# Optimization experiments

Measured on AMD Instinct MI355X. Metric: run time of the kernel, lower is better.

## Reference

```python
import jax, jax.numpy as jnp
import numpy as np

B, T, C, H = 4, 2048, 1024, 16


def setup_inputs() -> dict:
    key = jax.random.key(0)
    ks = jax.random.split(key, 5)
    s_attn = 1.0 / np.sqrt(C)
    s_proj = 1.0 / np.sqrt(C)
    return {
        "x": jax.random.normal(ks[0], (B, T, C), dtype=jnp.float32),
        "w_attn": jax.random.uniform(ks[1], (3 * C, C), dtype=jnp.float32, minval=-s_attn, maxval=s_attn),
        "b_attn": jax.random.uniform(ks[2], (3 * C,), dtype=jnp.float32, minval=-s_attn, maxval=s_attn),
        "w_proj": jax.random.uniform(ks[3], (C, C), dtype=jnp.float32, minval=-s_proj, maxval=s_proj),
        "b_proj": jax.random.uniform(ks[4], (C,), dtype=jnp.float32, minval=-s_proj, maxval=s_proj),
    }


def reference(x, w_attn, b_attn, w_proj, b_proj):
    b, t, c = x.shape
    hd = c // H  # head dim
    qkv = jnp.einsum('btc,dc->btd', x, w_attn) + b_attn  # [B,T,3C]
    q, k, v = jnp.split(qkv, 3, axis=-1)
    # [B,H,T,hd]
    q = q.reshape(b, t, H, hd).transpose(0, 2, 1, 3)
    k = k.reshape(b, t, H, hd).transpose(0, 2, 1, 3)
    v = v.reshape(b, t, H, hd).transpose(0, 2, 1, 3)
    att = jnp.einsum('bhqd,bhkd->bhqk', q, k) * (1.0 / np.sqrt(hd))
    mask = jnp.tril(jnp.ones((t, t), dtype=bool))  # causal
    att = jnp.where(mask, att, -jnp.inf)
    att = jax.nn.softmax(att, axis=-1)
    y = jnp.einsum('bhqk,bhkd->bhqd', att, v)
    y = y.transpose(0, 2, 1, 3).reshape(b, t, c)
    return jnp.einsum('btc,dc->btd', y, w_proj) + b_proj
```

## Files before the change

### kernel.cpp

```cpp
#include <hip/hip_runtime.h>

#define Bb 4
#define Tt 2048
#define Cc 1024
#define Hh 16
#define NQKV 3072
#define Mtot 8192

typedef __bf16 bf16_t;
typedef unsigned short u16;
typedef __bf16 bf16x8 __attribute__((ext_vector_type(8)));
typedef __bf16 bf16x4 __attribute__((ext_vector_type(4)));
typedef short short4v __attribute__((ext_vector_type(4)));
typedef float f32x4 __attribute__((ext_vector_type(4)));
typedef float f32x16 __attribute__((ext_vector_type(16)));
typedef unsigned uint2v __attribute__((ext_vector_type(2)));

union bfu { bf16_t b; u16 u; };
union trpair { short4v h[2]; bf16x8 v; };
union pfu { unsigned u[4]; bf16x8 v; };

#define QSCALE 0.18033688011112042f

#define TRD(dst, addr, OFF)                                                     \
  asm volatile("ds_read_b64_tr_b16 %0, %1 offset:" OFF                          \
               : "=v"(dst) : "v"(addr) : "memory")

__device__ __forceinline__ unsigned cvtpk(float a, float b) {
  unsigned r;
  asm("v_cvt_pk_bf16_f32 %0, %1, %2" : "=v"(r) : "v"(a), "v"(b));
  return r;
}
__device__ __forceinline__ uint2v plswap(unsigned a, unsigned b) {
  return __builtin_amdgcn_permlane32_swap(a, b, false, false);
}

__device__ __forceinline__ void cvt8(const float* s, u16* d, size_t i, float f) {
  float4 a = *(const float4*)(s + i);
  float4 b = *(const float4*)(s + i + 4);
  bf16x8 v;
  v[0]=(bf16_t)(a.x*f); v[1]=(bf16_t)(a.y*f); v[2]=(bf16_t)(a.z*f); v[3]=(bf16_t)(a.w*f);
  v[4]=(bf16_t)(b.x*f); v[5]=(bf16_t)(b.y*f); v[6]=(bf16_t)(b.z*f); v[7]=(bf16_t)(b.w*f);
  *(bf16x8*)(d + i) = v;
}

__global__ __launch_bounds__(256) void cvt_all(
    const float* __restrict__ x, const float* __restrict__ w_attn,
    const float* __restrict__ w_proj, const float* __restrict__ b_attn,
    u16* __restrict__ xb, u16* __restrict__ wab, u16* __restrict__ wpb,
    float* __restrict__ sbias)
{
  const int blk = blockIdx.x;
  if (blk < 4096) {
    size_t i = ((size_t)blk * 256 + threadIdx.x) * 8;
    cvt8(x, xb, i, 1.0f);
  } else if (blk < 5632) {
    size_t i = ((size_t)(blk - 4096) * 256 + threadIdx.x) * 8;
    cvt8(w_attn, wab, i, (i < (size_t)Cc * Cc) ? QSCALE : 1.0f);
  } else if (blk < 6144) {
    size_t i = ((size_t)(blk - 5632) * 256 + threadIdx.x) * 8;
    cvt8(w_proj, wpb, i, 1.0f);
  } else {
    int i0 = (blk - 6144) * 2048 + threadIdx.x * 8;
#pragma unroll
    for (int j = 0; j < 8; ++j) {
      int i = i0 + j;
      if (i < NQKV) sbias[i] = b_attn[i] * ((i < Cc) ? QSCALE : 1.0f);
    }
  }
}

template <int OUTBF16>
__global__ __launch_bounds__(256) void gemm_bf16(
    const u16* __restrict__ A, const u16* __restrict__ Bm,
    const float* __restrict__ bias, void* __restrict__ Cout,
    int M, int N, int K)
{
  __shared__ __attribute__((aligned(16))) u16 sa[128][40];
  __shared__ __attribute__((aligned(16))) u16 sb[128][40];

  const int tid  = threadIdx.x;
  const int lane = tid & 63;
  const int wid  = tid >> 6;
  const int wr   = (wid >> 1) * 64;
  const int wc   = (wid & 1) * 64;
  const int l15  = lane & 15;
  const int lh   = lane >> 4;
  const int bm   = blockIdx.x * 128;
  const int bn   = blockIdx.y * 128;

  f32x4 acc[4][4] = {};

  const int srow = tid >> 1;
  const int sseg = (tid & 1) * 16;

  const u16* pa = A  + (size_t)(bm + srow) * K + sseg;
  const u16* pb = Bm + (size_t)(bn + srow) * K + sseg;

  uint4 ar0 = *(const uint4*)pa, ar1 = *(const uint4*)(pa + 8);
  uint4 br0 = *(const uint4*)pb, br1 = *(const uint4*)(pb + 8);
  pa += 32; pb += 32;

  for (int k0 = 0; k0 < K; k0 += 32) {
    __syncthreads();
    *(uint4*)&sa[srow][sseg]     = ar0;
    *(uint4*)&sa[srow][sseg + 8] = ar1;
    *(uint4*)&sb[srow][sseg]     = br0;
    *(uint4*)&sb[srow][sseg + 8] = br1;
    __syncthreads();
    if (k0 + 32 < K) {
      ar0 = *(const uint4*)pa; ar1 = *(const uint4*)(pa + 8);
      br0 = *(const uint4*)pb; br1 = *(const uint4*)(pb + 8);
      pa += 32; pb += 32;
    }
    bf16x8 af[4], bfv[4];
#pragma unroll
    for (int mi = 0; mi < 4; mi++)
      af[mi] = *(const bf16x8*)&sa[wr + mi*16 + l15][lh * 8];
#pragma unroll
    for (int ni = 0; ni < 4; ni++)
      bfv[ni] = *(const bf16x8*)&sb[wc + ni*16 + l15][lh * 8];
#pragma unroll
    for (int mi = 0; mi < 4; mi++)
#pragma unroll
      for (int ni = 0; ni < 4; ni++)
        acc[mi][ni] = __builtin_amdgcn_mfma_f32_16x16x32_bf16(
            af[mi], bfv[ni], acc[mi][ni], 0, 0, 0);
  }

#pragma unroll
  for (int mi = 0; mi < 4; mi++) {
#pragma unroll
    for (int ni = 0; ni < 4; ni++) {
      const int col = bn + wc + ni*16 + l15;
      const float bs = bias[col];
#pragma unroll
      for (int r = 0; r < 4; r++) {
        const int row = bm + wr + mi*16 + lh*4 + r;
        const float val = acc[mi][ni][r] + bs;
        if (OUTBF16) {
          bfu cv; cv.b = (bf16_t)val;
          ((u16*)Cout)[(size_t)row * N + col] = cv.u;
        } else {
          ((float*)Cout)[(size_t)row * N + col] = val;
        }
      }
    }
  }
}

#define BUFU 9216

__global__ __launch_bounds__(512) void attn_kernel(
    const u16* __restrict__ qkv, u16* __restrict__ y)
{
  __shared__ __attribute__((aligned(16))) u16 smem[3 * BUFU];

  const int tid  = threadIdx.x;
  const int lane = tid & 63;
  const int w    = tid >> 6;
  const int l31  = lane & 31;
  const int hh   = lane >> 5;
  const int l15  = lane & 15;
  const int lh   = lane >> 4;
  const int bh   = blockIdx.y;
  const int b    = bh >> 4;
  const int head = bh & 15;

  const size_t rowbase = (size_t)b * Tt * NQKV;

  const int skey = tid >> 3;
  const int sp   = tid & 7;
  const u16* kbase = qkv + rowbase + 1024 + head*64 + sp*8;
  const u16* vbase = qkv + rowbase + 2048 + head*64 + sp*8;

  const unsigned smemB = (unsigned)(size_t)(&smem[0]);
  const unsigned trl = smemB
      + ((lh>>1)*8 + (l15>>2))*144 + (lh&1)*32 + (l15&3)*8;

  uint4 kr0, vr0;
#define LOADREGS(t) do {                                                        \
    kr0 = *(const uint4*)(kbase + (size_t)((t)*64 + skey) * NQKV);              \
    vr0 = *(const uint4*)(vbase + (size_t)((t)*64 + skey) * NQKV);              \
  } while (0)
#define STAGEB(bofs) do {                                                       \
    *(uint4*)&smem[(bofs) + skey*72 + sp*8]        = kr0;                       \
    *(uint4*)&smem[(bofs) + 4608 + skey*72 + sp*8] = vr0;                       \
  } while (0)

  for (int half = 0; half < 2; ++half) {
    const int qx    = half ? (7 - (int)blockIdx.x) : (int)blockIdx.x;
    const int qbase = qx * 256;
    const int qw    = qbase + w * 32;
    const int qi    = qw + l31;
    const int ktiles = 4*qx + 4;

    bf16x8 qfrag[4];
#pragma unroll
    for (int m = 0; m < 4; ++m)
      qfrag[m] = *(const bf16x8*)(qkv + rowbase + (size_t)qi * NQKV
                                  + head*64 + m*16 + hh*8);

    f32x16 o0 = {}, o1 = {};
    float m_run = -1e30f, l_part = 0.0f;
    f32x16 sA0, sA1, sB0, sB1;

    auto qk = [&](f32x16& t0, f32x16& t1, int kofs, int kb0) {
      f32x16 a0 = {}, a1 = {};
      __builtin_amdgcn_s_setprio(1);
#pragma unroll
      for (int m = 0; m < 4; ++m) {
        const int co = m*16 + hh*8;
        bf16x8 k0 = *(const bf16x8*)&smem[kofs + l31*72 + co];
        bf16x8 k1 = *(const bf16x8*)&smem[kofs + (32 + l31)*72 + co];
        a0 = __builtin_amdgcn_mfma_f32_32x32x16_bf16(k0, qfrag[m], a0, 0,0,0);
        a1 = __builtin_amdgcn_mfma_f32_32x32x16_bf16(k1, qfrag[m], a1, 0,0,0);
      }
      __builtin_amdgcn_s_setprio(0);
      if (kb0 + 63 > qw) {
#pragma unroll
        for (int r = 0; r < 16; ++r) {
          const int crow = (r&3) + 8*(r>>2) + 4*hh;
          if (kb0 + crow > qi)      a0[r] = -1e30f;
          if (kb0 + 32 + crow > qi) a1[r] = -1e30f;
        }
      }
      t0 = a0; t1 = a1;
    };

    auto smpv = [&](f32x16& s0, f32x16& s1, int bofs) {
      float mx[8];
#pragma unroll
      for (int i = 0; i < 8; ++i)
        mx[i] = fmaxf(fmaxf(s0[i], s0[i+8]), fmaxf(s1[i], s1[i+8]));
#pragma unroll
      for (int i = 0; i < 4; ++i) mx[i] = fmaxf(mx[i], mx[i+4]);
      mx[0] = fmaxf(mx[0], mx[2]); mx[1] = fmaxf(mx[1], mx[3]);
      float rm = fmaxf(mx[0], mx[1]);
      {
        uint2v t = plswap(__float_as_uint(rm), __float_as_uint(rm));
        rm = fmaxf(__uint_as_float(t[0]), __uint_as_float(t[1]));
      }
      if (__any(rm > m_run + 8.0f)) {
        const float mn = fmaxf(m_run, rm);
        const float al = exp2f(m_run - mn);
        m_run = mn; l_part *= al;
#pragma unroll
        for (int r = 0; r < 16; ++r) { o0[r] *= al; o1[r] *= al; }
      }

      pfu pf0, pf1, pf2, pf3;
      float lp0 = 0.f, lp1 = 0.f, lp2 = 0.f, lp3 = 0.f;
      {
        float pe[16];
#pragma unroll
        for (int r = 0; r < 16; ++r) pe[r] = exp2f(s0[r] - m_run);
#pragma unroll
        for (int r = 0; r < 4; ++r) {
          lp0 += pe[r]; lp1 += pe[4+r]; lp2 += pe[8+r]; lp3 += pe[12+r];
        }
        unsigned a0 = cvtpk(pe[0],pe[1]),  a1 = cvtpk(pe[2],pe[3]);
        unsigned a2 = cvtpk(pe[4],pe[5]),  a3 = cvtpk(pe[6],pe[7]);
        uint2v x1 = plswap(a0, a2), x2 = plswap(a1, a3);
        pf0.u[0]=x1[0]; pf0.u[1]=x2[0]; pf0.u[2]=x1[1]; pf0.u[3]=x2[1];
        unsigned b0 = cvtpk(pe[8],pe[9]),  b1 = cvtpk(pe[10],pe[11]);
        unsigned b2 = cvtpk(pe[12],pe[13]), b3 = cvtpk(pe[14],pe[15]);
        uint2v x3 = plswap(b0, b2), x4 = plswap(b1, b3);
        pf1.u[0]=x3[0]; pf1.u[1]=x4[0]; pf1.u[2]=x3[1]; pf1.u[3]=x4[1];
      }
      {
        float pe[16];
#pragma unroll
        for (int r = 0; r < 16; ++r) pe[r] = exp2f(s1[r] - m_run);
#pragma unroll
        for (int r = 0; r < 4; ++r) {
          lp0 += pe[r]; lp1 += pe[4+r]; lp2 += pe[8+r]; lp3 += pe[12+r];
        }
        unsigned a0 = cvtpk(pe[0],pe[1]),  a1 = cvtpk(pe[2],pe[3]);
        unsigned a2 = cvtpk(pe[4],pe[5]),  a3 = cvtpk(pe[6],pe[7]);
        uint2v x1 = plswap(a0, a2), x2 = plswap(a1, a3);
        pf2.u[0]=x1[0]; pf2.u[1]=x2[0]; pf2.u[2]=x1[1]; pf2.u[3]=x2[1];
        unsigned b0 = cvtpk(pe[8],pe[9]),  b1 = cvtpk(pe[10],pe[11]);
        unsigned b2 = cvtpk(pe[12],pe[13]), b3 = cvtpk(pe[14],pe[15]);
        uint2v x3 = plswap(b0, b2), x4 = plswap(b1, b3);
        pf3.u[0]=x3[0]; pf3.u[1]=x4[0]; pf3.u[2]=x3[1]; pf3.u[3]=x4[1];
      }
      l_part += (lp0 + lp1) + (lp2 + lp3);

      const unsigned va = trl + (unsigned)(bofs*2 + 9216);
      short4v ta0,tb0,ta1,tb1,ta2,tb2,ta3,tb3,ta4,tb4,ta5,tb5,ta6,tb6,ta7,tb7;
      TRD(ta0, va, "0");    TRD(tb0, va, "576");
      TRD(ta1, va, "64");   TRD(tb1, va, "640");
      TRD(ta2, va, "2304"); TRD(tb2, va, "2880");
      TRD(ta3, va, "2368"); TRD(tb3, va, "2944");
      TRD(ta4, va, "4608"); TRD(tb4, va, "5184");
      TRD(ta5, va, "4672"); TRD(tb5, va, "5248");
      TRD(ta6, va, "6912"); TRD(tb6, va, "7488");
      TRD(ta7, va, "6976"); TRD(tb7, va, "7552");
      asm volatile("s_waitcnt lgkmcnt(0)" ::: "memory");
      __builtin_amdgcn_sched_barrier(0);
      trpair v00,v01,v10,v11,v20,v21,v30,v31;
      v00.h[0]=ta0; v00.h[1]=tb0;  v01.h[0]=ta1; v01.h[1]=tb1;
      v10.h[0]=ta2; v10.h[1]=tb2;  v11.h[0]=ta3; v11.h[1]=tb3;
      v20.h[0]=ta4; v20.h[1]=tb4;  v21.h[0]=ta5; v21.h[1]=tb5;
      v30.h[0]=ta6; v30.h[1]=tb6;  v31.h[0]=ta7; v31.h[1]=tb7;
      __builtin_amdgcn_s_setprio(1);
      o0 = __builtin_amdgcn_mfma_f32_32x32x16_bf16(v00.v, pf0.v, o0, 0,0,0);
      o1 = __builtin_amdgcn_mfma_f32_32x32x16_bf16(v01.v, pf0.v, o1, 0,0,0);
      o0 = __builtin_amdgcn_mfma_f32_32x32x16_bf16(v10.v, pf1.v, o0, 0,0,0);
      o1 = __builtin_amdgcn_mfma_f32_32x32x16_bf16(v11.v, pf1.v, o1, 0,0,0);
      o0 = __builtin_amdgcn_mfma_f32_32x32x16_bf16(v20.v, pf2.v, o0, 0,0,0);
      o1 = __builtin_amdgcn_mfma_f32_32x32x16_bf16(v21.v, pf2.v, o1, 0,0,0);
      o0 = __builtin_amdgcn_mfma_f32_32x32x16_bf16(v30.v, pf3.v, o0, 0,0,0);
      o1 = __builtin_amdgcn_mfma_f32_32x32x16_bf16(v31.v, pf3.v, o1, 0,0,0);
      __builtin_amdgcn_s_setprio(0);
    };

    LOADREGS(0);
    __syncthreads();
    STAGEB(0);
    LOADREGS(1);
    __syncthreads();
    qk(sA0, sA1, 0, 0);
    STAGEB(BUFU);
    LOADREGS(2);

    int cofs = 0, nofs = BUFU, fofs = 2*BUFU;

    for (int kt = 0; kt < ktiles; kt += 2) {
      __syncthreads();
      if ((kt+1)*64 <= qw + 31) qk(sB0, sB1, nofs, (kt+1)*64);
      if (kt*64 <= qw + 31)     smpv(sA0, sA1, cofs);
      if (kt + 2 < ktiles) {
        STAGEB(fofs);
        if (kt + 3 < ktiles) LOADREGS(kt + 3);
      }
      { int t = cofs; cofs = nofs; nofs = fofs; fofs = t; }

      __syncthreads();
      if ((kt+2) < ktiles && (kt+2)*64 <= qw + 31) qk(sA0, sA1, nofs, (kt+2)*64);
      if ((kt+1)*64 <= qw + 31) smpv(sB0, sB1, cofs);
      if (kt + 3 < ktiles) {
        STAGEB(fofs);
        if (kt + 4 < ktiles) LOADREGS(kt + 4);
      }
      { int t = cofs; cofs = nofs; nofs = fofs; fofs = t; }
    }

    {
      uint2v t = plswap(__float_as_uint(l_part), __float_as_uint(l_part));
      l_part = __uint_as_float(t[0]) + __uint_as_float(t[1]);
    }
    const float inv = 1.0f / l_part;

    __syncthreads();
#pragma unroll
    for (int k4 = 0; k4 < 4; ++k4) {
      bf16x4 pa, pb;
#pragma unroll
      for (int j = 0; j < 4; ++j) {
        pa[j] = (bf16_t)(o0[4*k4 + j] * inv);
        pb[j] = (bf16_t)(o1[4*k4 + j] * inv);
      }
      *(bf16x4*)&smem[w*2304 + l31*72 +      8*k4 + 4*hh] = pa;
      *(bf16x4*)&smem[w*2304 + l31*72 + 32 + 8*k4 + 4*hh] = pb;
    }
    u16* yp = y + ((size_t)(b*Tt + qi)) * Cc + head*64;
#pragma unroll
    for (int p = 0; p < 4; ++p) {
      bf16x8 row = *(const bf16x8*)&smem[w*2304 + l31*72 + p*16 + hh*8];
      *(bf16x8*)(yp + p*16 + hh*8) = row;
    }
  }
#undef LOADREGS
#undef STAGEB
}

extern "C" void kernel_launch(void* const* d_in, const int* in_sizes, int n_in,
                              void* d_out, int out_size, void* d_ws, size_t ws_size,
                              hipStream_t stream) {
  const float* x      = (const float*)d_in[0];
  const float* w_attn = (const float*)d_in[1];
  const float* b_attn = (const float*)d_in[2];
  const float* w_proj = (const float*)d_in[3];
  const float* b_proj = (const float*)d_in[4];
  float* out = (float*)d_out;

  char* ws = (char*)d_ws;
  u16*   xb    = (u16*)(ws + 0);
  u16*   wab   = (u16*)(ws + 16777216);
  u16*   wpb   = (u16*)(ws + 23068672);
  u16*   qkvb  = (u16*)(ws + 25165824);
  u16*   yb    = (u16*)(ws + 75497472);
  float* sbias = (float*)(ws + 92274688);

  cvt_all<<<6146, 256, 0, stream>>>(x, w_attn, w_proj, b_attn,
                                    xb, wab, wpb, sbias);

  gemm_bf16<1><<<dim3(Mtot/128, NQKV/128), 256, 0, stream>>>(
      xb, wab, sbias, (void*)qkvb, Mtot, NQKV, Cc);

  attn_kernel<<<dim3(4, Bb*Hh), 512, 0, stream>>>(qkvb, yb);

  gemm_bf16<0><<<dim3(Mtot/128, Cc/128), 256, 0, stream>>>(
      yb, wpb, b_proj, (void*)out, Mtot, Cc, Cc);
}
```

Baseline: 181.8 us.

## Replace QKV GEMM with 256x256-tile kernel using direct-to-LDS double-buffered loads

```diff
diff --git a/kernel.cpp b/kernel.cpp
--- a/kernel.cpp
+++ b/kernel.cpp
@@ -34,6 +34,11 @@
 __device__ __forceinline__ uint2v plswap(unsigned a, unsigned b) {
   return __builtin_amdgcn_permlane32_swap(a, b, false, false);
 }
+
+#define GLOAD16(gsrc, ldst)                                                     \
+  __builtin_amdgcn_global_load_lds(                                             \
+      (const __attribute__((address_space(1))) unsigned int*)(gsrc),            \
+      (__attribute__((address_space(3))) unsigned int*)(ldst), 16, 0, 0)
 
 __device__ __forceinline__ void cvt8(const float* s, u16* d, size_t i, float f) {
   float4 a = *(const float4*)(s + i);
@@ -68,6 +73,90 @@
       if (i < NQKV) sbias[i] = b_attn[i] * ((i < Cc) ? QSCALE : 1.0f);
     }
   }
+}
+
+__global__ __launch_bounds__(512, 2) void gemm256(
+    const u16* __restrict__ A, const u16* __restrict__ Bm,
+    const float* __restrict__ bias, u16* __restrict__ Cout,
+    int M, int N, int K)
+{
+  __shared__ __attribute__((aligned(16))) u16 sa[2][8192];
+  __shared__ __attribute__((aligned(16))) u16 sb[2][8192];
+
+  const int tid  = threadIdx.x;
+  const int lane = tid & 63;
+  const int w    = tid >> 6;
+  const int wm   = w >> 2;
+  const int wn   = w & 3;
+  const int l15  = lane & 15;
+  const int lh   = lane >> 4;
+  const int bm   = blockIdx.x * 256;
+  const int bn   = blockIdx.y * 256;
+
+  f32x4 acc[8][4] = {};
+
+  const int sr = tid >> 2;
+  const int sc = (tid & 3) * 8;
+  const u16* pa0 = A  + (size_t)(bm + sr) * K + sc;
+  const u16* pa1 = A  + (size_t)(bm + 128 + sr) * K + sc;
+  const u16* pb0 = Bm + (size_t)(bn + sr) * K + sc;
+  const u16* pb1 = Bm + (size_t)(bn + 128 + sr) * K + sc;
+  const int d0 = tid * 8;
+
+#define STAGE_T(t, p) do {                                                      \
+    GLOAD16(pa0 + (size_t)(t) * 32, &sa[p][d0]);                                \
+    GLOAD16(pa1 + (size_t)(t) * 32, &sa[p][d0 + 4096]);                         \
+    GLOAD16(pb0 + (size_t)(t) * 32, &sb[p][d0]);                                \
+    GLOAD16(pb1 + (size_t)(t) * 32, &sb[p][d0 + 4096]);                         \
+  } while (0)
+
+  const int NT = K >> 5;
+  STAGE_T(0, 0);
+  STAGE_T(1, 1);
+
+  for (int t = 0; t < NT; ++t) {
+    const int p = t & 1;
+    if (t + 1 < NT) asm volatile("s_waitcnt vmcnt(4)" ::: "memory");
+    else            asm volatile("s_waitcnt vmcnt(0)" ::: "memory");
+    __builtin_amdgcn_s_barrier();
+    __builtin_amdgcn_sched_barrier(0);
+
+    bf16x8 bfr[4], afr[8];
+#pragma unroll
+    for (int nf = 0; nf < 4; ++nf)
+      bfr[nf] = *(const bf16x8*)&sb[p][(wn*64 + nf*16 + l15) * 32 + lh*8];
+#pragma unroll
+    for (int mf = 0; mf < 8; ++mf)
+      afr[mf] = *(const bf16x8*)&sa[p][(wm*128 + mf*16 + l15) * 32 + lh*8];
+
+    __builtin_amdgcn_s_setprio(1);
+#pragma unroll
+    for (int mf = 0; mf < 8; ++mf)
+#pragma unroll
+      for (int nf = 0; nf < 4; ++nf)
+        acc[mf][nf] = __builtin_amdgcn_mfma_f32_16x16x32_bf16(
+            afr[mf], bfr[nf], acc[mf][nf], 0, 0, 0);
+    __builtin_amdgcn_s_setprio(0);
+    __builtin_amdgcn_sched_barrier(0);
+    __builtin_amdgcn_s_barrier();
+    __builtin_amdgcn_sched_barrier(0);
+    if (t + 2 < NT) STAGE_T(t + 2, p);
+  }
+#undef STAGE_T
+
+#pragma unroll
+  for (int mf = 0; mf < 8; ++mf)
+#pragma unroll
+    for (int nf = 0; nf < 4; ++nf) {
+      const int col = bn + wn*64 + nf*16 + l15;
+      const float bs = bias[col];
+#pragma unroll
+      for (int r = 0; r < 4; ++r) {
+        const int row = bm + wm*128 + mf*16 + lh*4 + r;
+        bfu cv; cv.b = (bf16_t)(acc[mf][nf][r] + bs);
+        Cout[(size_t)row * N + col] = cv.u;
+      }
+    }
 }
 
 template <int OUTBF16>
@@ -397,8 +486,8 @@
   cvt_all<<<6146, 256, 0, stream>>>(x, w_attn, w_proj, b_attn,
                                     xb, wab, wpb, sbias);
 
-  gemm_bf16<1><<<dim3(Mtot/128, NQKV/128), 256, 0, stream>>>(
-      xb, wab, sbias, (void*)qkvb, Mtot, NQKV, Cc);
+  gemm256<<<dim3(Mtot/256, NQKV/256), 512, 0, stream>>>(
+      xb, wab, sbias, qkvb, Mtot, NQKV, Cc);
 
   attn_kernel<<<dim3(4, Bb*Hh), 512, 0, stream>>>(qkvb, yb);
 
```

Result: slower. 198.7 us (+9.3%).
